# Kernel optimization log

Measured on AMD Instinct MI355X. Metric: run time of the kernel, lower is better.

## Reference

```python
import jax, jax.numpy as jnp
import numpy as np

DIM = 1024
CTX_DIM = 1024
HEADS = 16
HEAD_DIM = DIM // HEADS


def setup_inputs() -> dict:
    key = jax.random.key(0)
    ks = jax.random.split(key, 6)
    B, N, M = 2, 2048, 2048
    s = 0.02
    return {
        "x": jax.random.normal(ks[0], (B, N, DIM), dtype=jnp.float32),
        "context": jax.random.normal(ks[1], (B, M, CTX_DIM), dtype=jnp.float32),
        "W_q": jax.random.normal(ks[2], (DIM, DIM), dtype=jnp.float32) * s,
        "W_kv": jax.random.normal(ks[3], (CTX_DIM * 2, CTX_DIM), dtype=jnp.float32) * s,
        "W_proj": jax.random.normal(ks[4], (DIM, DIM), dtype=jnp.float32) * s,
        "b_proj": jax.random.normal(ks[5], (DIM,), dtype=jnp.float32) * s,
    }


def reference(x, context, W_q, W_kv, W_proj, b_proj):
    B, N, C = x.shape
    M = context.shape[1]
    scale = HEAD_DIM ** (-0.5)
    # q projection: [B,N,H,D]
    q = (x @ W_q.T).reshape(B, N, HEADS, HEAD_DIM) * scale
    # context kv projection: [B,M,2,H,D]
    kv = (context @ W_kv.T).reshape(B, M, 2, HEADS, HEAD_DIM)
    k = kv[:, :, 0]  # [B,M,H,D]
    v = kv[:, :, 0]  # NOTE: source uses qkv_context[0] for BOTH k and v (faithful)
    attn = jnp.einsum("bnhd,bmhd->bhnm", q, k)
    attn = jax.nn.softmax(attn, axis=-1)
    out = jnp.einsum("bhnm,bmhd->bnhd", attn, v).reshape(B, N, C)
    return out @ W_proj.T + b_proj
```

## Files before the change

kernel.cpp:

```cpp
#include <hip/hip_runtime.h>
#include <hip/hip_bf16.h>


typedef __bf16 bf16x8 __attribute__((ext_vector_type(8)));
typedef float f32x4 __attribute__((ext_vector_type(4)));
typedef float f32x16 __attribute__((ext_vector_type(16)));

static constexpr int kDIM = 1024;
static constexpr float kLog2e = 1.4426950408889634f;

__device__ inline unsigned short f2bf(float f) {
    union { float f; unsigned int u; } v; v.f = f;
    return (unsigned short)((v.u + 0x7FFFu + ((v.u >> 16) & 1u)) >> 16);
}

__device__ inline unsigned int cvtpk2bf(float a, float b) {
    unsigned int r;
    asm("v_cvt_pk_bf16_f32 %0, %1, %2" : "=v"(r) : "v"(a), "v"(b));
    return r;
}

__device__ inline void gload_lds16(const unsigned short* g, unsigned short* l) {
    __builtin_amdgcn_global_load_lds(
        (const __attribute__((address_space(1))) unsigned int*)g,
        (__attribute__((address_space(3))) unsigned int*)l, 16, 0, 0);
}

__global__ __launch_bounds__(256) void cast_all(
    const float* __restrict__ x, const float* __restrict__ ctx,
    const float* __restrict__ wq, const float* __restrict__ wkv,
    const float* __restrict__ wp,
    unsigned short* __restrict__ xb, unsigned short* __restrict__ cb,
    unsigned short* __restrict__ wqb, unsigned short* __restrict__ wkb,
    unsigned short* __restrict__ wpb)
{
    int j = blockIdx.x * 256 + threadIdx.x;
    const float* s; unsigned short* d;
    if (j < 1048576)                      { s = x;   d = xb;  }
    else if ((j -= 1048576) < 1048576)    { s = ctx; d = cb;  }
    else if ((j -= 1048576) < 262144)     { s = wq;  d = wqb; }
    else if ((j -= 262144) < 262144)      { s = wkv; d = wkb; }
    else if ((j -= 262144) < 262144)      { s = wp;  d = wpb; }
    else return;
    float4 f = ((const float4*)s)[j];
    ushort4 o;
    o.x = f2bf(f.x); o.y = f2bf(f.y); o.z = f2bf(f.z); o.w = f2bf(f.w);
    ((ushort4*)d)[j] = o;
}

__global__ __launch_bounds__(512, 4) void gemm_qk(
    const unsigned short* __restrict__ xb, const unsigned short* __restrict__ cb,
    const unsigned short* __restrict__ Wq, const unsigned short* __restrict__ Wkv,
    unsigned short* __restrict__ Qb, unsigned short* __restrict__ Kb,
    unsigned short* __restrict__ Ktb, float qscale, int Mctx)
{
    __shared__ unsigned short As[2 * 128 * 64];
    __shared__ unsigned short Bs[2 * 128 * 64];
    const int z = blockIdx.z;
    const unsigned short* A  = z ? cb : xb;
    const unsigned short* Bw = z ? Wkv : Wq;
    unsigned short* Cb = z ? Kb : Qb;
    const float scale = z ? 1.0f : qscale;

    const int tid = threadIdx.x;
    const int wave = tid >> 6, lane = tid & 63;
    const int g = lane >> 4, c = lane & 15;
    const int wm = (wave >> 2) * 64, wn = (wave & 3) * 32;
    const int bm = blockIdx.y * 128, bn = blockIdx.x * 128;

    const int srow = lane >> 3;
    const int scolsw = ((lane & 7) ^ (srow & 7)) * 8;
    const int x7 = c & 7;

    f32x4 acc[4][2];
    #pragma unroll
    for (int i = 0; i < 4; ++i)
        #pragma unroll
        for (int j = 0; j < 2; ++j)
            acc[i][j] = (f32x4){0.f, 0.f, 0.f, 0.f};

    auto stage = [&](int buf, int k0) {
        unsigned short* Ad = As + buf * 8192;
        unsigned short* Bd = Bs + buf * 8192;
        #pragma unroll
        for (int t = 0; t < 2; ++t) {
            const int chunk = wave * 2 + t;
            gload_lds16(A + (size_t)(bm + chunk * 8 + srow) * kDIM + k0 + scolsw,
                        Ad + chunk * 512);
        }
        #pragma unroll
        for (int t = 0; t < 2; ++t) {
            const int chunk = wave * 2 + t;
            gload_lds16(Bw + (size_t)(bn + chunk * 8 + srow) * kDIM + k0 + scolsw,
                        Bd + chunk * 512);
        }
    };

    stage(0, 0);
    __syncthreads();

    for (int t = 0; t < 16; ++t) {
        const int cur = t & 1;
        if (t < 15) stage(cur ^ 1, (t + 1) * 64);
        const unsigned short* Ac = As + cur * 8192;
        const unsigned short* Bc = Bs + cur * 8192;
        #pragma unroll
        for (int kc = 0; kc < 2; ++kc) {
            bf16x8 af[4], bfr[2];
            #pragma unroll
            for (int i = 0; i < 4; ++i)
                af[i] = *(const bf16x8*)&Ac[(wm + i * 16 + c) * 64 +
                                            ((kc * 4 + g) ^ x7) * 8];
            #pragma unroll
            for (int j = 0; j < 2; ++j)
                bfr[j] = *(const bf16x8*)&Bc[(wn + j * 16 + c) * 64 +
                                             ((kc * 4 + g) ^ x7) * 8];
            #pragma unroll
            for (int i = 0; i < 4; ++i)
                #pragma unroll
                for (int j = 0; j < 2; ++j)
                    acc[i][j] = __builtin_amdgcn_mfma_f32_16x16x32_bf16(
                        af[i], bfr[j], acc[i][j], 0, 0, 0);
        }
        __syncthreads();
    }

    #pragma unroll
    for (int i = 0; i < 4; ++i) {
        #pragma unroll
        for (int j = 0; j < 2; ++j) {
            const int r0 = bm + wm + i * 16 + 4 * g;
            const int cc = bn + wn + j * 16 + c;
            float v0 = acc[i][j][0] * scale;
            float v1 = acc[i][j][1] * scale;
            float v2 = acc[i][j][2] * scale;
            float v3 = acc[i][j][3] * scale;
            Cb[(size_t)(r0 + 0) * kDIM + cc] = f2bf(v0);
            Cb[(size_t)(r0 + 1) * kDIM + cc] = f2bf(v1);
            Cb[(size_t)(r0 + 2) * kDIM + cc] = f2bf(v2);
            Cb[(size_t)(r0 + 3) * kDIM + cc] = f2bf(v3);
            if (z) {
                const int bb = r0 / Mctx, n0 = r0 % Mctx;
                const int hh = cc >> 6, d = cc & 63;
                ushort4 pk;
                pk.x = f2bf(v0); pk.y = f2bf(v1); pk.z = f2bf(v2); pk.w = f2bf(v3);
                *(ushort4*)&Ktb[((size_t)((bb * 16 + hh) * 64 + d)) * Mctx + n0] = pk;
            }
        }
    }
}

__global__ __launch_bounds__(256, 4) void gemm_proj(
    const unsigned short* __restrict__ Ab, const unsigned short* __restrict__ Wp,
    const float* __restrict__ bias, float* __restrict__ out)
{
    __shared__ unsigned short As[2 * 64 * 64];
    __shared__ unsigned short Bs[2 * 64 * 64];
    const int tid = threadIdx.x;
    const int wave = tid >> 6, lane = tid & 63;
    const int g = lane >> 4, c = lane & 15;
    const int wm = (wave & 1) * 32, wn = (wave >> 1) * 32;
    const int bm = blockIdx.y * 64, bn = blockIdx.x * 64;

    const int srow = lane >> 3;
    const int scolsw = ((lane & 7) ^ (srow & 7)) * 8;
    const int x7 = c & 7;

    f32x4 acc[2][2];
    #pragma unroll
    for (int i = 0; i < 2; ++i)
        #pragma unroll
        for (int j = 0; j < 2; ++j)
            acc[i][j] = (f32x4){0.f, 0.f, 0.f, 0.f};

    auto stage = [&](int buf, int k0) {
        unsigned short* Ad = As + buf * 4096;
        unsigned short* Bd = Bs + buf * 4096;
        #pragma unroll
        for (int t = 0; t < 2; ++t) {
            const int chunk = wave * 2 + t;
            const int row = chunk * 8 + srow;
            gload_lds16(Ab + (size_t)(bm + row) * kDIM + k0 + scolsw, Ad + chunk * 512);
            gload_lds16(Wp + (size_t)(bn + row) * kDIM + k0 + scolsw, Bd + chunk * 512);
        }
    };

    stage(0, 0);
    __syncthreads();

    for (int t = 0; t < 16; ++t) {
        const int cur = t & 1;
        if (t < 15) stage(cur ^ 1, (t + 1) * 64);
        const unsigned short* Ac = As + cur * 4096;
        const unsigned short* Bc = Bs + cur * 4096;
        #pragma unroll
        for (int kc = 0; kc < 2; ++kc) {
            bf16x8 af[2], bfr[2];
            #pragma unroll
            for (int i = 0; i < 2; ++i)
                af[i] = *(const bf16x8*)&Ac[(wm + i * 16 + c) * 64 +
                                            ((kc * 4 + g) ^ x7) * 8];
            #pragma unroll
            for (int j = 0; j < 2; ++j)
                bfr[j] = *(const bf16x8*)&Bc[(wn + j * 16 + c) * 64 +
                                             ((kc * 4 + g) ^ x7) * 8];
            #pragma unroll
            for (int i = 0; i < 2; ++i)
                #pragma unroll
                for (int j = 0; j < 2; ++j)
                    acc[i][j] = __builtin_amdgcn_mfma_f32_16x16x32_bf16(
                        af[i], bfr[j], acc[i][j], 0, 0, 0);
        }
        __syncthreads();
    }

    #pragma unroll
    for (int i = 0; i < 2; ++i) {
        #pragma unroll
        for (int j = 0; j < 2; ++j) {
            const int r0 = bm + wm + i * 16 + 4 * g;
            const int cc = bn + wn + j * 16 + c;
            const float bv = bias[cc];
            #pragma unroll
            for (int ii = 0; ii < 4; ++ii)
                out[(size_t)(r0 + ii) * kDIM + cc] = acc[i][j][ii] + bv;
        }
    }
}

__global__ __launch_bounds__(512, 4) void attn_mfma_v9(
    const unsigned short* __restrict__ Q,
    const unsigned short* __restrict__ K,
    const unsigned short* __restrict__ Kt,
    unsigned short* __restrict__ O, int N, int M)
{
    __shared__ unsigned short smem[18432];

    const int lin  = blockIdx.x + 16 * (blockIdx.y + 16 * blockIdx.z);
    const int orig = (lin & 7) * 64 + (lin >> 3);
    const int q0 = (orig & 15) * 128;
    const int h  = (orig >> 4) & 15;
    const int b  = orig >> 8;

    const int tid = threadIdx.x;
    const int w = tid >> 6, lane = tid & 63;
    const int strip = w >> 1, kh = w & 1;
    const int ql = lane & 31, l5 = lane >> 5;

    const unsigned short* Qrow = Q + (size_t)(b * N + q0 + strip * 32 + ql) * kDIM + h * 64;
    const unsigned short* Kb = K + (size_t)b * M * kDIM + h * 64;
    const unsigned short* Ktb = Kt + (size_t)((b * 16 + h) * 64) * M;

    bf16x8 bq[4];
    #pragma unroll
    for (int kc = 0; kc < 4; ++kc)
        bq[kc] = *(const bf16x8*)(Qrow + kc * 16 + l5 * 8);

    f32x16 ot[2];
    #pragma unroll
    for (int dt = 0; dt < 2; ++dt)
        #pragma unroll
        for (int r = 0; r < 16; ++r) ot[dt][r] = 0.f;
    float lac = 0.f;

    const int srow = tid >> 3, scol = (tid & 7) * 8;
    const int NT = M / 64;

    uint4 rk  = *(const uint4*)(Kb  + (size_t)srow * kDIM + scol);
    uint4 rkt = *(const uint4*)(Ktb + (size_t)srow * M + scol);
    *(uint4*)&smem[srow * 72 + scol]        = rk;
    *(uint4*)&smem[4608 + srow * 72 + scol] = rkt;
    rk  = *(const uint4*)(Kb  + (size_t)(64 + srow) * kDIM + scol);
    rkt = *(const uint4*)(Ktb + (size_t)srow * M + 64 + scol);
    __syncthreads();

    for (int t = 0; t < NT; ++t) {
        const int cur = t & 1;
        const unsigned short* Ksc  = smem + cur * 9216;
        const unsigned short* Ktsc = smem + cur * 9216 + 4608;

        if (t + 1 < NT) {
            unsigned short* Ksn = smem + (cur ^ 1) * 9216;
            *(uint4*)&Ksn[srow * 72 + scol]        = rk;
            *(uint4*)&Ksn[4608 + srow * 72 + scol] = rkt;
        }
        if (t + 2 < NT) {
            rk  = *(const uint4*)(Kb  + (size_t)((t + 2) * 64 + srow) * kDIM + scol);
            rkt = *(const uint4*)(Ktb + (size_t)srow * M + (t + 2) * 64 + scol);
        }

        f32x16 st;
        #pragma unroll
        for (int r = 0; r < 16; ++r) st[r] = 0.f;
        #pragma unroll
        for (int kc = 0; kc < 4; ++kc) {
            bf16x8 ak = *(const bf16x8*)&Ksc[(kh * 32 + ql) * 72 + kc * 16 + l5 * 8];
            st = __builtin_amdgcn_mfma_f32_32x32x16_bf16(ak, bq[kc], st, 0, 0, 0);
        }

        float pr[16];
        #pragma unroll
        for (int r = 0; r < 16; ++r) {
            pr[r] = __builtin_amdgcn_exp2f(st[r]);
            lac += pr[r];
        }
        unsigned int dw[8];
        #pragma unroll
        for (int p = 0; p < 8; ++p) dw[p] = cvtpk2bf(pr[2 * p], pr[2 * p + 1]);

        auto s02 = __builtin_amdgcn_permlane32_swap(dw[0], dw[2], false, false);
        auto s13 = __builtin_amdgcn_permlane32_swap(dw[1], dw[3], false, false);
        auto s46 = __builtin_amdgcn_permlane32_swap(dw[4], dw[6], false, false);
        auto s57 = __builtin_amdgcn_permlane32_swap(dw[5], dw[7], false, false);
        union BP { unsigned int u[4]; bf16x8 v; };
        BP b0, b1;
        b0.u[0] = s02[0]; b0.u[1] = s13[0]; b0.u[2] = s02[1]; b0.u[3] = s13[1];
        b1.u[0] = s46[0]; b1.u[1] = s57[0]; b1.u[2] = s46[1]; b1.u[3] = s57[1];
        bf16x8 bp[2] = { b0.v, b1.v };

        #pragma unroll
        for (int kc2 = 0; kc2 < 2; ++kc2) {
            #pragma unroll
            for (int dt = 0; dt < 2; ++dt) {
                bf16x8 av = *(const bf16x8*)&Ktsc[(dt * 32 + ql) * 72 + kh * 32 + kc2 * 16 + l5 * 8];
                ot[dt] = __builtin_amdgcn_mfma_f32_32x32x16_bf16(av, bp[kc2], ot[dt], 0, 0, 0);
            }
        }

        __syncthreads();
    }

    float lw = lac + __shfl_xor(lac, 32);
    float* Om = (float*)smem;
    float* Lm = Om + 128 * 68;
    const int qi = strip * 32 + ql;

    if (kh == 1) {
        #pragma unroll
        for (int dt = 0; dt < 2; ++dt)
            #pragma unroll
            for (int rr = 0; rr < 4; ++rr)
                *(f32x4*)&Om[qi * 68 + dt * 32 + 8 * rr + 4 * l5] =
                    (f32x4){ot[dt][4 * rr], ot[dt][4 * rr + 1],
                            ot[dt][4 * rr + 2], ot[dt][4 * rr + 3]};
        if (l5 == 0) Lm[qi] = lw;
    }
    __syncthreads();
    if (kh == 0) {
        const float inv = 1.0f / (lw + Lm[qi]);
        unsigned short* Ob = O + (size_t)(b * N + q0 + qi) * kDIM + h * 64;
        #pragma unroll
        for (int dt = 0; dt < 2; ++dt)
            #pragma unroll
            for (int rr = 0; rr < 4; ++rr) {
                f32x4 pv = *(const f32x4*)&Om[qi * 68 + dt * 32 + 8 * rr + 4 * l5];
                ushort4 u;
                u.x = f2bf((ot[dt][4 * rr]     + pv[0]) * inv);
                u.y = f2bf((ot[dt][4 * rr + 1] + pv[1]) * inv);
                u.z = f2bf((ot[dt][4 * rr + 2] + pv[2]) * inv);
                u.w = f2bf((ot[dt][4 * rr + 3] + pv[3]) * inv);
                *(ushort4*)(Ob + dt * 32 + 8 * rr + 4 * l5) = u;
            }
    }
}

extern "C" void kernel_launch(void* const* d_in, const int* in_sizes, int n_in,
                              void* d_out, int out_size, void* d_ws, size_t ws_size,
                              hipStream_t stream)
{
    const float* x      = (const float*)d_in[0];
    const float* ctxp   = (const float*)d_in[1];
    const float* W_q    = (const float*)d_in[2];
    const float* W_kv   = (const float*)d_in[3];
    const float* W_proj = (const float*)d_in[4];
    const float* b_proj = (const float*)d_in[5];
    float* out = (float*)d_out;

    const int B = 2, N = 2048, M = 2048;
    const int BN = B * N;
    const int SQ = kDIM * kDIM;

    unsigned short* p = (unsigned short*)d_ws;
    unsigned short* xb  = p; p += (size_t)BN * kDIM;
    unsigned short* cb  = p; p += (size_t)BN * kDIM;
    unsigned short* wqb = p; p += SQ;
    unsigned short* wkb = p; p += SQ;
    unsigned short* wpb = p; p += SQ;
    unsigned short* Qb  = p; p += (size_t)BN * kDIM;
    unsigned short* Kb  = p; p += (size_t)BN * kDIM;
    unsigned short* Ktb = p; p += (size_t)BN * kDIM;
    unsigned short* Ab  = xb;

    hipLaunchKernelGGL(cast_all, dim3(11264), dim3(256), 0, stream,
                       x, ctxp, W_q, W_kv, W_proj, xb, cb, wqb, wkb, wpb);
    hipLaunchKernelGGL(gemm_qk, dim3(kDIM / 128, BN / 128, 2), dim3(512), 0, stream,
                       xb, cb, wqb, wkb, Qb, Kb, Ktb, 0.125f * kLog2e, M);
    hipLaunchKernelGGL(attn_mfma_v9, dim3(N / 128, 16, B), dim3(512), 0, stream,
                       Qb, Kb, Ktb, Ab, N, M);
    hipLaunchKernelGGL(gemm_proj, dim3(kDIM / 64, BN / 64), dim3(256), 0, stream,
                       Ab, wpb, b_proj, out);
}
```

Measured before the change: 183.9 us.

## Single-buffer GEMM tiles, widen proj K-tile, add MFMA priority hints in attention

The Q/K projection GEMM drops double-buffered LDS staging for a single buffer with a barrier before and after each load. The output-projection GEMM goes to a single buffer with a 128-wide K tile and a 16-way XOR swizzle, halving its loop trip count. The attention kernel wraps its MFMA sections in s_setprio raises so waves issuing matrix ops get scheduling priority over waves doing exp/convert work. Less LDS per block may allow more resident blocks, but removing double buffering exposes global-load latency that is no longer hidden behind compute.

New measurement: 177.5 us. 1.04x faster.

```diff
diff --git a/kernel.cpp b/kernel.cpp
--- a/kernel.cpp
+++ b/kernel.cpp
@@ -54,8 +54,8 @@
     unsigned short* __restrict__ Qb, unsigned short* __restrict__ Kb,
     unsigned short* __restrict__ Ktb, float qscale, int Mctx)
 {
-    __shared__ unsigned short As[2 * 128 * 64];
-    __shared__ unsigned short Bs[2 * 128 * 64];
+    __shared__ unsigned short As[128 * 64];
+    __shared__ unsigned short Bs[128 * 64];
     const int z = blockIdx.z;
     const unsigned short* A  = z ? cb : xb;
     const unsigned short* Bw = z ? Wkv : Wq;
@@ -79,41 +79,31 @@
         for (int j = 0; j < 2; ++j)
             acc[i][j] = (f32x4){0.f, 0.f, 0.f, 0.f};
 
-    auto stage = [&](int buf, int k0) {
-        unsigned short* Ad = As + buf * 8192;
-        unsigned short* Bd = Bs + buf * 8192;
+    for (int k0 = 0; k0 < kDIM; k0 += 64) {
+        __syncthreads();
         #pragma unroll
         for (int t = 0; t < 2; ++t) {
             const int chunk = wave * 2 + t;
             gload_lds16(A + (size_t)(bm + chunk * 8 + srow) * kDIM + k0 + scolsw,
-                        Ad + chunk * 512);
+                        &As[chunk * 512]);
         }
         #pragma unroll
         for (int t = 0; t < 2; ++t) {
             const int chunk = wave * 2 + t;
             gload_lds16(Bw + (size_t)(bn + chunk * 8 + srow) * kDIM + k0 + scolsw,
-                        Bd + chunk * 512);
-        }
-    };
-
-    stage(0, 0);
-    __syncthreads();
-
-    for (int t = 0; t < 16; ++t) {
-        const int cur = t & 1;
-        if (t < 15) stage(cur ^ 1, (t + 1) * 64);
-        const unsigned short* Ac = As + cur * 8192;
-        const unsigned short* Bc = Bs + cur * 8192;
+                        &Bs[chunk * 512]);
+        }
+        __syncthreads();
         #pragma unroll
         for (int kc = 0; kc < 2; ++kc) {
             bf16x8 af[4], bfr[2];
             #pragma unroll
             for (int i = 0; i < 4; ++i)
-                af[i] = *(const bf16x8*)&Ac[(wm + i * 16 + c) * 64 +
+                af[i] = *(const bf16x8*)&As[(wm + i * 16 + c) * 64 +
                                             ((kc * 4 + g) ^ x7) * 8];
             #pragma unroll
             for (int j = 0; j < 2; ++j)
-                bfr[j] = *(const bf16x8*)&Bc[(wn + j * 16 + c) * 64 +
+                bfr[j] = *(const bf16x8*)&Bs[(wn + j * 16 + c) * 64 +
                                              ((kc * 4 + g) ^ x7) * 8];
             #pragma unroll
             for (int i = 0; i < 4; ++i)
@@ -122,7 +112,6 @@
                     acc[i][j] = __builtin_amdgcn_mfma_f32_16x16x32_bf16(
                         af[i], bfr[j], acc[i][j], 0, 0, 0);
         }
-        __syncthreads();
     }
 
     #pragma unroll
@@ -154,17 +143,17 @@
     const unsigned short* __restrict__ Ab, const unsigned short* __restrict__ Wp,
     const float* __restrict__ bias, float* __restrict__ out)
 {
-    __shared__ unsigned short As[2 * 64 * 64];
-    __shared__ unsigned short Bs[2 * 64 * 64];
+    __shared__ unsigned short As[64 * 128];
+    __shared__ unsigned short Bs[64 * 128];
     const int tid = threadIdx.x;
     const int wave = tid >> 6, lane = tid & 63;
     const int g = lane >> 4, c = lane & 15;
     const int wm = (wave & 1) * 32, wn = (wave >> 1) * 32;
     const int bm = blockIdx.y * 64, bn = blockIdx.x * 64;
 
-    const int srow = lane >> 3;
-    const int scolsw = ((lane & 7) ^ (srow & 7)) * 8;
-    const int x7 = c & 7;
+    const int srow = lane >> 4;
+    const int scg  = lane & 15;
+    const int x15 = c & 15;
 
     f32x4 acc[2][2];
     #pragma unroll
@@ -173,37 +162,28 @@
         for (int j = 0; j < 2; ++j)
             acc[i][j] = (f32x4){0.f, 0.f, 0.f, 0.f};
 
-    auto stage = [&](int buf, int k0) {
-        unsigned short* Ad = As + buf * 4096;
-        unsigned short* Bd = Bs + buf * 4096;
-        #pragma unroll
-        for (int t = 0; t < 2; ++t) {
-            const int chunk = wave * 2 + t;
-            const int row = chunk * 8 + srow;
-            gload_lds16(Ab + (size_t)(bm + row) * kDIM + k0 + scolsw, Ad + chunk * 512);
-            gload_lds16(Wp + (size_t)(bn + row) * kDIM + k0 + scolsw, Bd + chunk * 512);
-        }
-    };
-
-    stage(0, 0);
-    __syncthreads();
-
-    for (int t = 0; t < 16; ++t) {
-        const int cur = t & 1;
-        if (t < 15) stage(cur ^ 1, (t + 1) * 64);
-        const unsigned short* Ac = As + cur * 4096;
-        const unsigned short* Bc = Bs + cur * 4096;
-        #pragma unroll
-        for (int kc = 0; kc < 2; ++kc) {
+    for (int k0 = 0; k0 < kDIM; k0 += 128) {
+        __syncthreads();
+        #pragma unroll
+        for (int t = 0; t < 4; ++t) {
+            const int chunk = wave * 4 + t;
+            const int row = chunk * 4 + srow;
+            const int scol = (scg ^ (row & 15)) * 8;
+            gload_lds16(Ab + (size_t)(bm + row) * kDIM + k0 + scol, &As[chunk * 512]);
+            gload_lds16(Wp + (size_t)(bn + row) * kDIM + k0 + scol, &Bs[chunk * 512]);
+        }
+        __syncthreads();
+        #pragma unroll
+        for (int kk = 0; kk < 4; ++kk) {
             bf16x8 af[2], bfr[2];
             #pragma unroll
             for (int i = 0; i < 2; ++i)
-                af[i] = *(const bf16x8*)&Ac[(wm + i * 16 + c) * 64 +
-                                            ((kc * 4 + g) ^ x7) * 8];
+                af[i] = *(const bf16x8*)&As[(wm + i * 16 + c) * 128 +
+                                            ((kk * 4 + g) ^ x15) * 8];
             #pragma unroll
             for (int j = 0; j < 2; ++j)
-                bfr[j] = *(const bf16x8*)&Bc[(wn + j * 16 + c) * 64 +
-                                             ((kc * 4 + g) ^ x7) * 8];
+                bfr[j] = *(const bf16x8*)&Bs[(wn + j * 16 + c) * 128 +
+                                             ((kk * 4 + g) ^ x15) * 8];
             #pragma unroll
             for (int i = 0; i < 2; ++i)
                 #pragma unroll
@@ -211,7 +191,6 @@
                     acc[i][j] = __builtin_amdgcn_mfma_f32_16x16x32_bf16(
                         af[i], bfr[j], acc[i][j], 0, 0, 0);
         }
-        __syncthreads();
     }
 
     #pragma unroll
@@ -292,11 +271,13 @@
         f32x16 st;
         #pragma unroll
         for (int r = 0; r < 16; ++r) st[r] = 0.f;
+        __builtin_amdgcn_s_setprio(1);
         #pragma unroll
         for (int kc = 0; kc < 4; ++kc) {
             bf16x8 ak = *(const bf16x8*)&Ksc[(kh * 32 + ql) * 72 + kc * 16 + l5 * 8];
             st = __builtin_amdgcn_mfma_f32_32x32x16_bf16(ak, bq[kc], st, 0, 0, 0);
         }
+        __builtin_amdgcn_s_setprio(0);
 
         float pr[16];
         #pragma unroll
@@ -318,6 +299,7 @@
         b1.u[0] = s46[0]; b1.u[1] = s57[0]; b1.u[2] = s46[1]; b1.u[3] = s57[1];
         bf16x8 bp[2] = { b0.v, b1.v };
 
+        __builtin_amdgcn_s_setprio(1);
         #pragma unroll
         for (int kc2 = 0; kc2 < 2; ++kc2) {
             #pragma unroll
@@ -326,6 +308,7 @@
                 ot[dt] = __builtin_amdgcn_mfma_f32_32x32x16_bf16(av, bp[kc2], ot[dt], 0, 0, 0);
             }
         }
+        __builtin_amdgcn_s_setprio(0);
 
         __syncthreads();
     }
```
